# Optimization experiments

Measured on AMD Instinct MI355X. Metric: run time of the kernel, lower is better.

The kernel has to match this reference:

```python
import jax, jax.numpy as jnp
import numpy as np

EMBED_DIM = 512
NUM_HEADS = 8
HEAD_DIM = EMBED_DIM // NUM_HEADS
FACTOR = 5
B, T = 4, 2048


def setup_inputs() -> dict:
    key = jax.random.key(0)
    ks = jax.random.split(key, 10)
    s = EMBED_DIM ** -0.5
    hidden_states = jax.random.normal(ks[0], (B, T, EMBED_DIM), dtype=jnp.float32)
    log_L = int(np.ceil(np.log1p(T)))
    u_part = min(FACTOR * T * log_L, T)
    index_sample = jax.random.randint(ks[1], (u_part,), 0, T, dtype=jnp.int32)
    Wq = jax.random.normal(ks[2], (EMBED_DIM, EMBED_DIM), dtype=jnp.float32) * s
    bq = jnp.zeros((EMBED_DIM,), dtype=jnp.float32)
    Wk = jax.random.normal(ks[3], (EMBED_DIM, EMBED_DIM), dtype=jnp.float32) * s
    bk = jnp.zeros((EMBED_DIM,), dtype=jnp.float32)
    Wv = jax.random.normal(ks[4], (EMBED_DIM, EMBED_DIM), dtype=jnp.float32) * s
    bv = jnp.zeros((EMBED_DIM,), dtype=jnp.float32)
    Wo = jax.random.normal(ks[5], (EMBED_DIM, EMBED_DIM), dtype=jnp.float32) * s
    bo = jnp.zeros((EMBED_DIM,), dtype=jnp.float32)
    return {"hidden_states": hidden_states, "index_sample": index_sample,
            "Wq": Wq, "bq": bq, "Wk": Wk, "bk": bk, "Wv": Wv, "bv": bv,
            "Wo": Wo, "bo": bo}


def _split_heads(x, bsz, seqlen):
    # [B, T, E] -> [B*H, T, head_dim]
    return x.reshape(bsz, seqlen, NUM_HEADS, HEAD_DIM).transpose(0, 2, 1, 3).reshape(bsz * NUM_HEADS, seqlen, HEAD_DIM)


def reference(hidden_states, index_sample, Wq, bq, Wk, bk, Wv, bv, Wo, bo):
    bsz, tgt_len, embed_dim = hidden_states.shape
    scaling = HEAD_DIM ** -0.5
    q = (hidden_states @ Wq.T + bq) * scaling
    k = hidden_states @ Wk.T + bk
    v = hidden_states @ Wv.T + bv
    q = _split_heads(q, bsz, tgt_len)   # [BH, T, d]
    k = _split_heads(k, bsz, tgt_len)
    v = _split_heads(v, bsz, tgt_len)
    L_k = tgt_len
    log_q = int(np.ceil(np.log1p(tgt_len)))
    u = min(FACTOR * log_q, tgt_len)
    # random key sampling (indices precomputed, length u_part)
    k_sample = k[:, index_sample, :]                                  # [BH, u_part, d]
    qk_sample = jnp.einsum('bqd,bkd->bqk', q, k_sample)               # [BH, T, u_part]
    # sparsity measurement: max - mean over sampled keys (mean uses full L_k as in source)
    sparsity = qk_sample.max(axis=-1) - qk_sample.sum(axis=-1) / L_k  # [BH, T]
    top_idx = jax.lax.top_k(sparsity, u)[1]                           # [BH, u]
    q_reduce = jnp.take_along_axis(q, top_idx[:, :, None], axis=1)    # [BH, u, d]
    attn = jax.nn.softmax(jnp.einsum('bud,bkd->buk', q_reduce, k), axis=-1)  # [BH, u, L]
    attn_out = jnp.einsum('buk,bkd->bud', attn, v)                    # [BH, u, d]
    # encoder context: mean of values over time, scattered with active-query outputs
    context = jnp.broadcast_to(v.mean(axis=1, keepdims=True), v.shape)  # [BH, T, d]
    bh_idx = jnp.arange(bsz * NUM_HEADS)[:, None]
    context = context.at[bh_idx, top_idx].set(attn_out)
    out = context.reshape(bsz, NUM_HEADS, tgt_len, HEAD_DIM).transpose(0, 2, 1, 3).reshape(bsz, tgt_len, embed_dim)
    return out @ Wo.T + bo
```

## Files before the change

kernel.cpp:

```cpp
#include <hip/hip_runtime.h>
#include <hip/hip_bf16.h>
#include <math.h>

#define T_LEN 2048
#define EMB   512
#define NHEAD 8
#define HDIM  64
#define BHEADS 32
#define USEL  40

typedef __bf16 bf16v8 __attribute__((ext_vector_type(8)));
typedef _Float16 f16x8 __attribute__((ext_vector_type(8)));
typedef float f32x4 __attribute__((ext_vector_type(4)));
typedef unsigned short u16;

__device__ __forceinline__ void cvt4_hilo(const float4 f, uint2& ph, uint2& pl)
{
    __hip_bfloat16 h0 = __float2bfloat16(f.x);
    __hip_bfloat16 h1 = __float2bfloat16(f.y);
    __hip_bfloat16 h2 = __float2bfloat16(f.z);
    __hip_bfloat16 h3 = __float2bfloat16(f.w);
    __hip_bfloat16 l0 = __float2bfloat16(f.x - __bfloat162float(h0));
    __hip_bfloat16 l1 = __float2bfloat16(f.y - __bfloat162float(h1));
    __hip_bfloat16 l2 = __float2bfloat16(f.z - __bfloat162float(h2));
    __hip_bfloat16 l3 = __float2bfloat16(f.w - __bfloat162float(h3));
    ph.x = (unsigned)*(const u16*)&h0 | ((unsigned)*(const u16*)&h1 << 16);
    ph.y = (unsigned)*(const u16*)&h2 | ((unsigned)*(const u16*)&h3 << 16);
    pl.x = (unsigned)*(const u16*)&l0 | ((unsigned)*(const u16*)&l1 << 16);
    pl.y = (unsigned)*(const u16*)&l2 | ((unsigned)*(const u16*)&l3 << 16);
}

__device__ __forceinline__ void cvt4_hilo_h(const float4 f, uint2& ph, uint2& pl)
{
    _Float16 h0 = (_Float16)f.x;
    _Float16 h1 = (_Float16)f.y;
    _Float16 h2 = (_Float16)f.z;
    _Float16 h3 = (_Float16)f.w;
    _Float16 l0 = (_Float16)(f.x - (float)h0);
    _Float16 l1 = (_Float16)(f.y - (float)h1);
    _Float16 l2 = (_Float16)(f.z - (float)h2);
    _Float16 l3 = (_Float16)(f.w - (float)h3);
    ph.x = (unsigned)*(const u16*)&h0 | ((unsigned)*(const u16*)&h1 << 16);
    ph.y = (unsigned)*(const u16*)&h2 | ((unsigned)*(const u16*)&h3 << 16);
    pl.x = (unsigned)*(const u16*)&l0 | ((unsigned)*(const u16*)&l1 << 16);
    pl.y = (unsigned)*(const u16*)&l2 | ((unsigned)*(const u16*)&l3 << 16);
}

__device__ __forceinline__ void cvt1_hilo_h(float f, u16& h, u16& l)
{
    _Float16 hh = (_Float16)f;
    _Float16 ll = (_Float16)(f - (float)hh);
    h = *(const u16*)&hh;
    l = *(const u16*)&ll;
}

__global__ __launch_bounds__(256)
void pack_hilo_kernel(const float* __restrict__ X,
                      const float* __restrict__ Wq, const float* __restrict__ Wk,
                      const float* __restrict__ Wv, const float* __restrict__ Wo,
                      u16* __restrict__ Xp, u16* __restrict__ Wp)
{
    alignas(16) __shared__ u16 th[4096];
    alignas(16) __shared__ u16 tl[4096];
    const int b = blockIdx.x, tid = threadIdx.x;

    const float* src; u16* dst;
    if (b < 1024) {
        int mt = b >> 4, kt = b & 15;
        src = X + (size_t)(mt * 128) * EMB + kt * 32;
        dst = Xp + (size_t)b * 8192;
    } else {
        int wdx = b - 1024;
        int z = wdx >> 6, nt = (wdx >> 4) & 3, kt = wdx & 15;
        const float* W = (z == 0) ? Wq : (z == 1) ? Wk : (z == 2) ? Wv : Wo;
        src = W + (size_t)(nt * 128) * EMB + kt * 32;
        dst = Wp + (size_t)wdx * 8192;
    }

    #pragma unroll
    for (int s = 0; s < 4; ++s) {
        int u = tid + 256 * s;
        int row = u >> 3, c4 = u & 7;
        float4 f = *(const float4*)&src[(size_t)row * EMB + c4 * 4];
        uint2 ph, pl;
        cvt4_hilo_h(f, ph, pl);
        int kq = c4 >> 1, e4 = (c4 & 1) * 4;
        *(uint2*)&th[kq * 1024 + row * 8 + e4] = ph;
        *(uint2*)&tl[kq * 1024 + row * 8 + e4] = pl;
    }
    __syncthreads();

    uint4* d4 = (uint4*)dst;
    const uint4* s4h = (const uint4*)th;
    const uint4* s4l = (const uint4*)tl;
    d4[tid]       = s4h[tid];
    d4[tid + 256] = s4h[tid + 256];
    d4[tid + 512] = s4l[tid];
    d4[tid + 768] = s4l[tid + 256];
}

__global__ __launch_bounds__(256)
void qkv_mfma_kernel(const u16* __restrict__ Xp, const u16* __restrict__ Wp,
                     const float* __restrict__ bq, const float* __restrict__ bk,
                     const float* __restrict__ bv,
                     float* __restrict__ qo, float* __restrict__ ko, float* __restrict__ vo)
{
    alignas(16) __shared__ u16 Ah[2][4096];
    alignas(16) __shared__ u16 Al[2][4096];
    alignas(16) __shared__ u16 Bh[2][4096];
    alignas(16) __shared__ u16 Bl[2][4096];

    const int z = blockIdx.z;
    const float* bias; float* dst; float scale;
    if (z == 0)      { bias = bq; dst = qo; scale = 0.125f; }
    else if (z == 1) { bias = bk; dst = ko; scale = 1.0f;   }
    else             { bias = bv; dst = vo; scale = 1.0f;   }
    const bool three = (z != 2);

    const int tid = threadIdx.x;
    const int mt = blockIdx.x;
    const int nt = blockIdx.y;
    const int w = tid >> 6, lane = tid & 63;
    const int wm = w & 1, wn = w >> 1;
    const int lm = lane & 15, kq = lane >> 4;

    const u16* Abase = Xp + (size_t)mt * (16 * 8192);
    const u16* Bbase = Wp + (size_t)(z * 4 + nt) * (16 * 8192);

    f32x4 acc[4][4];
    #pragma unroll
    for (int i = 0; i < 4; ++i)
        #pragma unroll
        for (int j = 0; j < 4; ++j)
            #pragma unroll
            for (int r = 0; r < 4; ++r) acc[i][j][r] = 0.0f;

    auto stage = [&](int kt, int buf) {
        const u16* at = Abase + kt * 8192;
        const u16* bt = Bbase + kt * 8192;
        const u16* gsrc; u16* ldst;
        if (w == 0)      { gsrc = at;        ldst = &Ah[buf][0]; }
        else if (w == 1) { gsrc = at + 4096; ldst = &Al[buf][0]; }
        else if (w == 2) { gsrc = bt;        ldst = &Bh[buf][0]; }
        else             { gsrc = bt + 4096; ldst = &Bl[buf][0]; }
        if (three || (w & 1) == 0) {
            #pragma unroll
            for (int i = 0; i < 8; ++i)
                __builtin_amdgcn_global_load_lds(
                    (const __attribute__((address_space(1))) void*)(gsrc + (size_t)lane * 8 + i * 512),
                    (__attribute__((address_space(3))) void*)(ldst + i * 512),
                    16, 0, 0);
        }
    };

    stage(0, 0);

    for (int kt = 0; kt < 16; ++kt) {
        const int cur = kt & 1;
        if (kt + 1 < 16) {
            stage(kt + 1, cur ^ 1);
            asm volatile("s_waitcnt vmcnt(8)" ::: "memory");
        } else {
            asm volatile("s_waitcnt vmcnt(0)" ::: "memory");
        }
        __builtin_amdgcn_s_barrier();
        __builtin_amdgcn_sched_barrier(0);

        f16x8 ah[4], al[4], bh[4], bl[4];
        #pragma unroll
        for (int i = 0; i < 4; ++i) {
            int ar = (wm * 64 + i * 16 + lm) * 8 + kq * 1024;
            int br = (wn * 64 + i * 16 + lm) * 8 + kq * 1024;
            ah[i] = *(const f16x8*)&Ah[cur][ar];
            bh[i] = *(const f16x8*)&Bh[cur][br];
            if (three) {
                al[i] = *(const f16x8*)&Al[cur][ar];
                bl[i] = *(const f16x8*)&Bl[cur][br];
            }
        }
        #pragma unroll
        for (int i = 0; i < 4; ++i)
            #pragma unroll
            for (int j = 0; j < 4; ++j) {
                acc[i][j] = __builtin_amdgcn_mfma_f32_16x16x32_f16(ah[i], bh[j], acc[i][j], 0, 0, 0);
                if (three) {
                    acc[i][j] = __builtin_amdgcn_mfma_f32_16x16x32_f16(ah[i], bl[j], acc[i][j], 0, 0, 0);
                    acc[i][j] = __builtin_amdgcn_mfma_f32_16x16x32_f16(al[i], bh[j], acc[i][j], 0, 0, 0);
                }
            }
        __builtin_amdgcn_s_barrier();
    }

    #pragma unroll
    for (int j = 0; j < 4; ++j) {
        int ng = nt * 128 + wn * 64 + j * 16 + lm;
        int h = ng >> 6, d = ng & 63;
        float bv_ = bias[ng];
        #pragma unroll
        for (int i = 0; i < 4; ++i) {
            #pragma unroll
            for (int r = 0; r < 4; ++r) {
                int mg = mt * 128 + wm * 64 + i * 16 + kq * 4 + r;
                int b = mg >> 11, t = mg & 2047;
                dst[((size_t)((b * NHEAD + h) * T_LEN + t)) * HDIM + d] =
                    (acc[i][j][r] + bv_) * scale;
            }
        }
    }
}

__global__ __launch_bounds__(256)
void qkv_proj_kernel(const float* __restrict__ X,
                     const float* __restrict__ Wq, const float* __restrict__ bq,
                     const float* __restrict__ Wk, const float* __restrict__ bk,
                     const float* __restrict__ Wv, const float* __restrict__ bv,
                     float* __restrict__ qo, float* __restrict__ ko, float* __restrict__ vo)
{
    alignas(16) __shared__ u16 Ah[128 * 40];
    alignas(16) __shared__ u16 Al[128 * 40];
    alignas(16) __shared__ u16 Bh[128 * 40];
    alignas(16) __shared__ u16 Bl[128 * 40];

    const int z = blockIdx.z;
    const float* W; const float* bias; float* dst; float scale;
    if (z == 0)      { W = Wq; bias = bq; dst = qo; scale = 0.125f; }
    else if (z == 1) { W = Wk; bias = bk; dst = ko; scale = 1.0f;   }
    else             { W = Wv; bias = bv; dst = vo; scale = 1.0f;   }

    const int tid = threadIdx.x;
    const int m0 = blockIdx.x * 128;
    const int n0 = blockIdx.y * 128;
    const int w = tid >> 6, lane = tid & 63;
    const int wm = w & 1, wn = w >> 1;
    const int lm = lane & 15, kq = lane >> 4;

    f32x4 acc[4][4];
    #pragma unroll
    for (int i = 0; i < 4; ++i)
        #pragma unroll
        for (int j = 0; j < 4; ++j)
            #pragma unroll
            for (int r = 0; r < 4; ++r) acc[i][j][r] = 0.0f;

    for (int kc = 0; kc < EMB; kc += 32) {
        __syncthreads();
        #pragma unroll
        for (int s = 0; s < 4; ++s) {
            int u = tid + 256 * s;
            int row = u >> 3, c4 = u & 7;
            float4 fa = *(const float4*)&X[(size_t)(m0 + row) * EMB + kc + c4 * 4];
            float4 fb = *(const float4*)&W[(n0 + row) * EMB + kc + c4 * 4];
            uint2 ph, pl;
            cvt4_hilo_h(fa, ph, pl);
            *(uint2*)&Ah[row * 40 + c4 * 4] = ph;
            *(uint2*)&Al[row * 40 + c4 * 4] = pl;
            cvt4_hilo_h(fb, ph, pl);
            *(uint2*)&Bh[row * 40 + c4 * 4] = ph;
            *(uint2*)&Bl[row * 40 + c4 * 4] = pl;
        }
        __syncthreads();

        f16x8 ah[4], al[4], bh[4], bl[4];
        #pragma unroll
        for (int i = 0; i < 4; ++i) {
            int ra = (wm * 64 + i * 16 + lm) * 40 + kq * 8;
            ah[i] = *(const f16x8*)&Ah[ra];
            al[i] = *(const f16x8*)&Al[ra];
            int rb = (wn * 64 + i * 16 + lm) * 40 + kq * 8;
            bh[i] = *(const f16x8*)&Bh[rb];
            bl[i] = *(const f16x8*)&Bl[rb];
        }
        #pragma unroll
        for (int i = 0; i < 4; ++i)
            #pragma unroll
            for (int j = 0; j < 4; ++j) {
                acc[i][j] = __builtin_amdgcn_mfma_f32_16x16x32_f16(ah[i], bh[j], acc[i][j], 0, 0, 0);
                acc[i][j] = __builtin_amdgcn_mfma_f32_16x16x32_f16(ah[i], bl[j], acc[i][j], 0, 0, 0);
                acc[i][j] = __builtin_amdgcn_mfma_f32_16x16x32_f16(al[i], bh[j], acc[i][j], 0, 0, 0);
            }
    }

    #pragma unroll
    for (int j = 0; j < 4; ++j) {
        int ng = n0 + wn * 64 + j * 16 + lm;
        int h = ng >> 6, d = ng & 63;
        float bv_ = bias[ng];
        #pragma unroll
        for (int i = 0; i < 4; ++i) {
            #pragma unroll
            for (int r = 0; r < 4; ++r) {
                int mg = m0 + wm * 64 + i * 16 + kq * 4 + r;
                int b = mg >> 11, t = mg & 2047;
                dst[((size_t)((b * NHEAD + h) * T_LEN + t)) * HDIM + d] =
                    (acc[i][j][r] + bv_) * scale;
            }
        }
    }
}

__global__ __launch_bounds__(256)
void count_compact_kernel(const int* __restrict__ idxs, int n,
                          int* __restrict__ count, int* __restrict__ klist,
                          int* __restrict__ ncp)
{
    __shared__ int cnt[T_LEN];
    __shared__ int th_tot[256];
    __shared__ int th_off[256];
    __shared__ int ncs;
    const int tid = threadIdx.x;
    for (int j = tid; j < T_LEN; j += 256) cnt[j] = 0;
    __syncthreads();
    for (int i = tid; i < n; i += 256) atomicAdd(&cnt[idxs[i] & (T_LEN - 1)], 1);
    __syncthreads();
    const int base = tid * 8;
    int flags[8]; int loc = 0;
    #pragma unroll
    for (int j = 0; j < 8; ++j) {
        int c = cnt[base + j];
        count[base + j] = c;
        flags[j] = (c > 0); loc += flags[j];
    }
    th_tot[tid] = loc;
    __syncthreads();
    if (tid == 0) {
        int run = 0;
        for (int i = 0; i < 256; ++i) { th_off[i] = run; run += th_tot[i]; }
        ncs = run;
        ncp[0] = run;
    }
    __syncthreads();
    int off = th_off[tid];
    #pragma unroll
    for (int j = 0; j < 8; ++j)
        if (flags[j]) klist[off++] = base + j;
    __syncthreads();
    const int nc = ncs;
    const int nt = (nc + 127) & ~127;
    const int k0 = klist[0];
    for (int j = nc + tid; j < nt; j += 256) klist[j] = k0;
}

__global__ __launch_bounds__(256)
void ksum_vmean_part_kernel(const int* __restrict__ count,
                            const float* __restrict__ k, const float* __restrict__ v,
                            float* __restrict__ kpart, float* __restrict__ vpart)
{
    __shared__ int cs[256];
    alignas(16) __shared__ float rk[16 * 64];
    alignas(16) __shared__ float rv[16 * 64];

    const int sl = blockIdx.x, bh = blockIdx.y, tid = threadIdx.x;
    const int f4 = tid & 15, tg = tid >> 4;
    const int t0 = sl * 256;

    cs[tid] = count[t0 + tid];
    __syncthreads();

    const float4* k4 = (const float4*)(k + (size_t)bh * T_LEN * HDIM) + t0 * 16;
    const float4* v4 = (const float4*)(v + (size_t)bh * T_LEN * HDIM) + t0 * 16;

    float4 ak = {0.f, 0.f, 0.f, 0.f}, av = {0.f, 0.f, 0.f, 0.f};
    #pragma unroll
    for (int s = 0; s < 16; ++s) {
        int t = tg + s * 16;
        float c = (float)cs[t];
        float4 kf = k4[t * 16 + f4];
        float4 vf = v4[t * 16 + f4];
        ak.x = fmaf(c, kf.x, ak.x); ak.y = fmaf(c, kf.y, ak.y);
        ak.z = fmaf(c, kf.z, ak.z); ak.w = fmaf(c, kf.w, ak.w);
        av.x += vf.x; av.y += vf.y; av.z += vf.z; av.w += vf.w;
    }
    *(float4*)&rk[tg * 64 + f4 * 4] = ak;
    *(float4*)&rv[tg * 64 + f4 * 4] = av;
    __syncthreads();

    if (tid < 64) {
        float sk = 0.f, sv = 0.f;
        #pragma unroll
        for (int g = 0; g < 16; ++g) { sk += rk[g * 64 + tid]; sv += rv[g * 64 + tid]; }
        kpart[((size_t)bh * 8 + sl) * 64 + tid] = sk;
        vpart[((size_t)bh * 8 + sl) * 64 + tid] = sv;
    }
}

__global__ __launch_bounds__(64)
void ksum_vmean_reduce_kernel(const float* __restrict__ kpart, const float* __restrict__ vpart,
                              float* __restrict__ ksum, float* __restrict__ vmean)
{
    const int bh = blockIdx.x, d = threadIdx.x;
    float sk = 0.f, sv = 0.f;
    #pragma unroll
    for (int sl = 0; sl < 8; ++sl) {
        sk += kpart[((size_t)bh * 8 + sl) * 64 + d];
        sv += vpart[((size_t)bh * 8 + sl) * 64 + d];
    }
    ksum[bh * 64 + d]  = sk;
    vmean[bh * 64 + d] = sv * (1.0f / 2048.0f);
}

__global__ __launch_bounds__(256)
void pack_k_kernel(const float* __restrict__ k, const int* __restrict__ klist,
                   const int* __restrict__ ncp, u16* __restrict__ Kp)
{
    alignas(16) __shared__ u16 th[8192];
    alignas(16) __shared__ u16 tl[8192];
    const int wg = blockIdx.x, tid = threadIdx.x;
    const int swz = (wg & 7) * 64 + (wg >> 3);
    const int bh = swz >> 4, kt = swz & 15;
    const int ntiles = (ncp[0] + 127) >> 7;
    if (kt >= ntiles) return;

    const float4* kb4 = (const float4*)(k + (size_t)bh * T_LEN * HDIM);
    #pragma unroll
    for (int s = 0; s < 8; ++s) {
        int u = tid + 256 * s;
        int row = u >> 4, c4 = u & 15;
        int krow = klist[kt * 128 + row];
        float4 f = kb4[krow * 16 + c4];
        uint2 ph, pl;
        cvt4_hilo_h(f, ph, pl);
        int base = (c4 >> 3) * 4096 + ((c4 >> 1) & 3) * 1024 + row * 8 + (c4 & 1) * 4;
        *(uint2*)&th[base] = ph;
        *(uint2*)&tl[base] = pl;
    }
    __syncthreads();

    u16* dst = Kp + ((size_t)bh * 16 + kt) * 16384;
    uint4* d4 = (uint4*)dst;
    const uint4* s4h = (const uint4*)th;
    const uint4* s4l = (const uint4*)tl;
    #pragma unroll
    for (int i = 0; i < 4; ++i) d4[tid + 256 * i] = s4h[tid + 256 * i];
    #pragma unroll
    for (int i = 0; i < 4; ++i) d4[1024 + tid + 256 * i] = s4l[tid + 256 * i];
}

__global__ __launch_bounds__(256)
void sparsity_scan_kernel(const float* __restrict__ q, const u16* __restrict__ Kp,
                          const float* __restrict__ ksum,
                          const int* __restrict__ ncp, float* __restrict__ spars)
{
    alignas(16) __shared__ u16 KH[10240];
    alignas(16) __shared__ u16 KL[10240];
    __shared__ float ksm[64];
    __shared__ float smax[128];
    __shared__ float sdotL[128];

    const int tid = threadIdx.x;
    const int wg = blockIdx.x;
    const int swz = (wg & 7) * 64 + (wg >> 3);
    const int bh = swz >> 4;
    const int q0 = (swz & 15) * 128;
    const int w = tid >> 6, lane = tid & 63;
    const int lm = lane & 15, kq = lane >> 4;

    const float* qb = q + ((size_t)bh * T_LEN + q0) * HDIM;
    const int ntiles = (ncp[0] + 127) >> 7;

    if (tid < 64) ksm[tid] = ksum[bh * 64 + tid];

    #pragma unroll
    for (int s = 0; s < 8; ++s) {
        int u = tid + 256 * s;
        int row = u >> 4, c4 = u & 15;
        float4 f = *(const float4*)&qb[row * HDIM + c4 * 4];
        uint2 ph, pl;
        cvt4_hilo_h(f, ph, pl);
        int base = ((c4 >> 3) * 128 + row) * 40 + (c4 & 7) * 4;
        *(uint2*)&KH[base] = ph;
        *(uint2*)&KL[base] = pl;
    }
    __syncthreads();

    f16x8 qh[2][2], ql[2][2];
    #pragma unroll
    for (int i = 0; i < 2; ++i)
        #pragma unroll
        for (int c = 0; c < 2; ++c) {
            int ra = (c * 128 + w * 32 + i * 16 + lm) * 40 + kq * 8;
            qh[i][c] = *(const f16x8*)&KH[ra];
            ql[i][c] = *(const f16x8*)&KL[ra];
        }

    {
        float4 k0a = *(const float4*)&ksm[kq * 8];
        float4 k0b = *(const float4*)&ksm[kq * 8 + 4];
        float4 k1a = *(const float4*)&ksm[32 + kq * 8];
        float4 k1b = *(const float4*)&ksm[32 + kq * 8 + 4];
        float kmv[2][8] = {{k0a.x, k0a.y, k0a.z, k0a.w, k0b.x, k0b.y, k0b.z, k0b.w},
                           {k1a.x, k1a.y, k1a.z, k1a.w, k1b.x, k1b.y, k1b.z, k1b.w}};
        #pragma unroll
        for (int i = 0; i < 2; ++i) {
            float sd = 0.f;
            #pragma unroll
            for (int c = 0; c < 2; ++c)
                #pragma unroll
                for (int e = 0; e < 8; ++e)
                    sd = fmaf((float)qh[i][c][e] + (float)ql[i][c][e], kmv[c][e], sd);
            sd += __shfl_xor(sd, 16, 64);
            sd += __shfl_xor(sd, 32, 64);
            if (kq == 0) sdotL[w * 32 + i * 16 + lm] = sd;
        }
    }

    float vmax[2][4];
    #pragma unroll
    for (int i = 0; i < 2; ++i)
        #pragma unroll
        for (int r = 0; r < 4; ++r) vmax[i][r] = -INFINITY;

    const u16* kpb = Kp + (size_t)bh * (16 * 16384);

    for (int kt = 0; kt < ntiles; ++kt) {
        __syncthreads();
        const u16* kp = kpb + kt * 16384;
        const u16* gsrc; u16* ldst;
        if (w == 0)      { gsrc = kp;         ldst = KH; }
        else if (w == 1) { gsrc = kp + 4096;  ldst = KH + 4096; }
        else if (w == 2) { gsrc = kp + 8192;  ldst = KL; }
        else             { gsrc = kp + 12288; ldst = KL + 4096; }
        #pragma unroll
        for (int i = 0; i < 8; ++i)
            __builtin_amdgcn_global_load_lds(
                (const __attribute__((address_space(1))) void*)(gsrc + (size_t)lane * 8 + i * 512),
                (__attribute__((address_space(3))) void*)(ldst + i * 512),
                16, 0, 0);
        __syncthreads();

        #pragma unroll
        for (int j = 0; j < 8; ++j) {
            int rb0 = kq * 1024 + (j * 16 + lm) * 8;
            int rb1 = 4096 + kq * 1024 + (j * 16 + lm) * 8;
            f16x8 bh0 = *(const f16x8*)&KH[rb0];
            f16x8 bl0 = *(const f16x8*)&KL[rb0];
            f16x8 bh1 = *(const f16x8*)&KH[rb1];
            f16x8 bl1 = *(const f16x8*)&KL[rb1];
            f32x4 a0 = {0.f, 0.f, 0.f, 0.f};
            f32x4 a1 = {0.f, 0.f, 0.f, 0.f};
            a0 = __builtin_amdgcn_mfma_f32_16x16x32_f16(qh[0][0], bh0, a0, 0, 0, 0);
            a1 = __builtin_amdgcn_mfma_f32_16x16x32_f16(qh[1][0], bh0, a1, 0, 0, 0);
            a0 = __builtin_amdgcn_mfma_f32_16x16x32_f16(qh[0][0], bl0, a0, 0, 0, 0);
            a1 = __builtin_amdgcn_mfma_f32_16x16x32_f16(qh[1][0], bl0, a1, 0, 0, 0);
            a0 = __builtin_amdgcn_mfma_f32_16x16x32_f16(ql[0][0], bh0, a0, 0, 0, 0);
            a1 = __builtin_amdgcn_mfma_f32_16x16x32_f16(ql[1][0], bh0, a1, 0, 0, 0);
            a0 = __builtin_amdgcn_mfma_f32_16x16x32_f16(qh[0][1], bh1, a0, 0, 0, 0);
            a1 = __builtin_amdgcn_mfma_f32_16x16x32_f16(qh[1][1], bh1, a1, 0, 0, 0);
            a0 = __builtin_amdgcn_mfma_f32_16x16x32_f16(qh[0][1], bl1, a0, 0, 0, 0);
            a1 = __builtin_amdgcn_mfma_f32_16x16x32_f16(qh[1][1], bl1, a1, 0, 0, 0);
            a0 = __builtin_amdgcn_mfma_f32_16x16x32_f16(ql[0][1], bh1, a0, 0, 0, 0);
            a1 = __builtin_amdgcn_mfma_f32_16x16x32_f16(ql[1][1], bh1, a1, 0, 0, 0);
            #pragma unroll
            for (int r = 0; r < 4; ++r) {
                vmax[0][r] = fmaxf(vmax[0][r], a0[r]);
                vmax[1][r] = fmaxf(vmax[1][r], a1[r]);
            }
        }
    }

    #pragma unroll
    for (int i = 0; i < 2; ++i)
        #pragma unroll
        for (int r = 0; r < 4; ++r) {
            float m = vmax[i][r];
            m = fmaxf(m, __shfl_xor(m, 1, 64));
            m = fmaxf(m, __shfl_xor(m, 2, 64));
            m = fmaxf(m, __shfl_xor(m, 4, 64));
            m = fmaxf(m, __shfl_xor(m, 8, 64));
            if (lm == 0) smax[w * 32 + i * 16 + kq * 4 + r] = m;
        }
    __syncthreads();

    if (tid < 128)
        spars[bh * T_LEN + q0 + tid] = smax[tid] - sdotL[tid] * (1.0f / 2048.0f);
}

__global__ __launch_bounds__(256)
void sparsity_scan_fb_kernel(const float* __restrict__ q, const float* __restrict__ k,
                             const float* __restrict__ ksum, const int* __restrict__ klist,
                             const int* __restrict__ ncp, float* __restrict__ spars)
{
    alignas(16) __shared__ u16 KH[256 * 40];
    alignas(16) __shared__ u16 KL[256 * 40];
    __shared__ float ksm[64];
    __shared__ float smax[128];
    __shared__ float sdotL[128];

    const int tid = threadIdx.x;
    const int bh = blockIdx.y;
    const int q0 = blockIdx.x * 128;
    const int w = tid >> 6, lane = tid & 63;
    const int lm = lane & 15, kq = lane >> 4;

    const float* qb = q + ((size_t)bh * T_LEN + q0) * HDIM;
    const float4* kb4 = (const float4*)(k + (size_t)bh * T_LEN * HDIM);
    const int ntiles = (ncp[0] + 127) >> 7;

    if (tid < 64) ksm[tid] = ksum[bh * 64 + tid];

    #pragma unroll
    for (int s = 0; s < 8; ++s) {
        int u = tid + 256 * s;
        int row = u >> 4, c4 = u & 15;
        float4 f = *(const float4*)&qb[row * HDIM + c4 * 4];
        uint2 ph, pl;
        cvt4_hilo_h(f, ph, pl);
        int base = ((c4 >> 3) * 128 + row) * 40 + (c4 & 7) * 4;
        *(uint2*)&KH[base] = ph;
        *(uint2*)&KL[base] = pl;
    }
    __syncthreads();

    f16x8 qh[2][2], ql[2][2];
// ... 141 lines not shown
        const int A = (tid == 255) ? 0 : sfx[tid + 1];
        const int here = sfx[tid];
        __syncthreads();
        if (A < need && here >= need) {
            sh_bin = tid;
            sh_need = need - A;
        }
        __syncthreads();
        kpref |= (unsigned)sh_bin << shift;
        shift -= 8;
    }

    const unsigned K = kpref;
    const int need_eq = sh_need;

    #pragma unroll
    for (int s = 0; s < 8; ++s) {
        int j = tid + 256 * s;
        unsigned kk = keys[j];
        if (kk > K) {
            int pos = atomicAdd(&nsel, 1);
            if (pos < USEL) topi[bh * USEL + pos] = j;
        } else if (kk == K) {
            atomicAdd(&neq, 1);
        }
    }
    __syncthreads();
    const int base = nsel;
    const int E = neq;
    __syncthreads();

    if (E == need_eq) {
        #pragma unroll
        for (int s = 0; s < 8; ++s) {
            int j = tid + 256 * s;
            if (keys[j] == K) {
                int pos = atomicAdd(&cnt2, 1);
                if (base + pos < USEL) topi[bh * USEL + base + pos] = j;
            }
        }
    } else {
        #pragma unroll
        for (int s = 0; s < 8; ++s) {
            int j = tid + 256 * s;
            if (keys[j] == K) {
                int rank = 0;
                for (int j2 = 0; j2 < j; ++j2) rank += (keys[j2] == K);
                if (rank < need_eq && base + rank < USEL)
                    topi[bh * USEL + base + rank] = j;
            }
        }
    }
}

__global__ __launch_bounds__(256)
void gather_q_kernel(const float* __restrict__ q, const int* __restrict__ topi,
                     float* __restrict__ qsel)
{
    const int bh = blockIdx.x, tid = threadIdx.x;
    for (int i = tid; i < USEL * HDIM; i += 256) {
        int u = i >> 6, d = i & 63;
        int t = topi[bh * USEL + u] & (T_LEN - 1);
        qsel[(size_t)bh * USEL * HDIM + i] = q[((size_t)bh * T_LEN + t) * HDIM + d];
    }
}

__global__ __launch_bounds__(256)
void sel_scores_direct_kernel(const float* __restrict__ q, const float* __restrict__ k,
                              const int* __restrict__ topi, float* __restrict__ S)
{
    __shared__ float qsT[64 * 41];
    __shared__ float ksT[64 * 257];

    const int sl = blockIdx.x, bh = blockIdx.y, tid = threadIdx.x;
    const int t0 = sl * 256;

    for (int i = tid; i < USEL * HDIM; i += 256) {
        int u = i >> 6, d = i & 63;
        int t = topi[bh * USEL + u] & (T_LEN - 1);
        qsT[d * 41 + u] = q[((size_t)bh * T_LEN + t) * HDIM + d];
    }
    const float4* k4 = (const float4*)(k + (size_t)bh * T_LEN * HDIM);
    #pragma unroll
    for (int s = 0; s < 16; ++s) {
        int u = tid + 256 * s;
        int c4 = u & 15, t = u >> 4;
        float4 f = k4[(t0 + t) * 16 + c4];
        ksT[(c4 * 4 + 0) * 257 + t] = f.x;
        ksT[(c4 * 4 + 1) * 257 + t] = f.y;
        ksT[(c4 * 4 + 2) * 257 + t] = f.z;
        ksT[(c4 * 4 + 3) * 257 + t] = f.w;
    }
    __syncthreads();

    const int qg = tid >> 5;
    const int kg = tid & 31;

    float acc[5][8];
    #pragma unroll
    for (int i = 0; i < 5; ++i)
        #pragma unroll
        for (int j = 0; j < 8; ++j) acc[i][j] = 0.0f;

    #pragma unroll 4
    for (int d = 0; d < 64; ++d) {
        float qv[5], kv[8];
        #pragma unroll
        for (int i = 0; i < 5; ++i) qv[i] = qsT[d * 41 + qg * 5 + i];
        #pragma unroll
        for (int j = 0; j < 8; ++j) kv[j] = ksT[d * 257 + kg + 32 * j];
        #pragma unroll
        for (int i = 0; i < 5; ++i)
            #pragma unroll
            for (int j = 0; j < 8; ++j)
                acc[i][j] = fmaf(qv[i], kv[j], acc[i][j]);
    }

    #pragma unroll
    for (int i = 0; i < 5; ++i) {
        float* sp = &S[((size_t)bh * USEL + qg * 5 + i) * T_LEN + t0 + kg];
        #pragma unroll
        for (int j = 0; j < 8; ++j) sp[32 * j] = acc[i][j];
    }
}

__global__ __launch_bounds__(256)
void sel_scores_kernel(const float* __restrict__ qsel, const float* __restrict__ k,
                       float* __restrict__ S)
{
    __shared__ float qsT[64 * 41];
    __shared__ float ksT[64 * 257];

    const int sl = blockIdx.x, bh = blockIdx.y, tid = threadIdx.x;
    const int t0 = sl * 256;

    for (int i = tid; i < USEL * HDIM; i += 256) {
        int u = i >> 6, d = i & 63;
        qsT[d * 41 + u] = qsel[(size_t)bh * USEL * HDIM + i];
    }
    const float4* k4 = (const float4*)(k + (size_t)bh * T_LEN * HDIM);
    #pragma unroll
    for (int s = 0; s < 16; ++s) {
        int u = tid + 256 * s;
        int c4 = u & 15, t = u >> 4;
        float4 f = k4[(t0 + t) * 16 + c4];
        ksT[(c4 * 4 + 0) * 257 + t] = f.x;
        ksT[(c4 * 4 + 1) * 257 + t] = f.y;
        ksT[(c4 * 4 + 2) * 257 + t] = f.z;
        ksT[(c4 * 4 + 3) * 257 + t] = f.w;
    }
    __syncthreads();

    const int qg = tid >> 5;
    const int kg = tid & 31;

    float acc[5][8];
    #pragma unroll
    for (int i = 0; i < 5; ++i)
        #pragma unroll
        for (int j = 0; j < 8; ++j) acc[i][j] = 0.0f;

    #pragma unroll 4
    for (int d = 0; d < 64; ++d) {
        float qv[5], kv[8];
        #pragma unroll
        for (int i = 0; i < 5; ++i) qv[i] = qsT[d * 41 + qg * 5 + i];
        #pragma unroll
        for (int j = 0; j < 8; ++j) kv[j] = ksT[d * 257 + kg + 32 * j];
        #pragma unroll
        for (int i = 0; i < 5; ++i)
            #pragma unroll
            for (int j = 0; j < 8; ++j)
                acc[i][j] = fmaf(qv[i], kv[j], acc[i][j]);
    }

    #pragma unroll
    for (int i = 0; i < 5; ++i) {
        float* sp = &S[((size_t)bh * USEL + qg * 5 + i) * T_LEN + t0 + kg];
        #pragma unroll
        for (int j = 0; j < 8; ++j) sp[32 * j] = acc[i][j];
    }
}

__global__ __launch_bounds__(256)
void sel_softmax_kernel(float* __restrict__ S)
{
    __shared__ float red[256];
    const int row = blockIdx.x, tid = threadIdx.x;
    float* sr = S + (size_t)row * T_LEN;

    float x[8];
    float m = -INFINITY;
    #pragma unroll
    for (int s = 0; s < 8; ++s) { x[s] = sr[tid + 256 * s]; m = fmaxf(m, x[s]); }
    red[tid] = m;
    __syncthreads();
    for (int s = 128; s > 0; s >>= 1) {
        if (tid < s) red[tid] = fmaxf(red[tid], red[tid + s]);
        __syncthreads();
    }
    m = red[0];
    __syncthreads();

    float sum = 0.f;
    #pragma unroll
    for (int s = 0; s < 8; ++s) { x[s] = __expf(x[s] - m); sum += x[s]; }
    red[tid] = sum;
    __syncthreads();
    for (int s = 128; s > 0; s >>= 1) {
        if (tid < s) red[tid] += red[tid + s];
        __syncthreads();
    }
    float inv = 1.0f / red[0];
    #pragma unroll
    for (int s = 0; s < 8; ++s) sr[tid + 256 * s] = x[s] * inv;
}

__global__ __launch_bounds__(256)
void pv_part_kernel(const float* __restrict__ S, const float* __restrict__ v,
                    float* __restrict__ part)
{
    __shared__ float ps[USEL * 128];
    __shared__ float vs[128 * 69];
    __shared__ float obuf[128 * 20];

    const int sl = blockIdx.x, bh = blockIdx.y, tid = threadIdx.x;
    const int t0 = sl * 128;

    for (int i = tid; i < USEL * 128; i += 256) {
        int q = i >> 7, t = i & 127;
        ps[q * 128 + t] = S[((size_t)bh * USEL + q) * T_LEN + t0 + t];
    }
    const float4* v4 = (const float4*)(v + (size_t)bh * T_LEN * HDIM);
    #pragma unroll
    for (int s = 0; s < 8; ++s) {
        int u = tid + 256 * s;
        int c4 = u & 15, t = u >> 4;
        float4 f = v4[(t0 + t) * 16 + c4];
        vs[t * 69 + c4 * 4 + 0] = f.x;
        vs[t * 69 + c4 * 4 + 1] = f.y;
        vs[t * 69 + c4 * 4 + 2] = f.z;
        vs[t * 69 + c4 * 4 + 3] = f.w;
    }
    __syncthreads();

    const int qg = tid >> 5, r = tid & 31;
    const int dg = r >> 1, th = r & 1;
    const int tb = th * 64;

    float o[5][4];
    #pragma unroll
    for (int i = 0; i < 5; ++i)
        #pragma unroll
        for (int j = 0; j < 4; ++j) o[i][j] = 0.0f;

    #pragma unroll 4
    for (int tt = 0; tt < 64; ++tt) {
        int t = tb + tt;
        float pv[5];
        #pragma unroll
        for (int i = 0; i < 5; ++i) pv[i] = ps[(qg * 5 + i) * 128 + t];
        float4 vv = *(const float4*)&vs[t * 69 + dg * 4];
        #pragma unroll
        for (int i = 0; i < 5; ++i) {
            o[i][0] = fmaf(pv[i], vv.x, o[i][0]);
            o[i][1] = fmaf(pv[i], vv.y, o[i][1]);
            o[i][2] = fmaf(pv[i], vv.z, o[i][2]);
            o[i][3] = fmaf(pv[i], vv.w, o[i][3]);
        }
    }

    const int p = qg * 16 + dg;
    if (th == 1) {
        #pragma unroll
        for (int i = 0; i < 5; ++i)
            #pragma unroll
            for (int j = 0; j < 4; ++j) obuf[p * 20 + i * 4 + j] = o[i][j];
    }
    __syncthreads();
    if (th == 0) {
        float* pb = part + ((size_t)bh * 16 + sl) * (USEL * HDIM);
        #pragma unroll
        for (int i = 0; i < 5; ++i)
            #pragma unroll
            for (int j = 0; j < 4; ++j)
                pb[(qg * 5 + i) * HDIM + dg * 4 + j] = o[i][j] + obuf[p * 20 + i * 4 + j];
    }
}

__global__ __launch_bounds__(256)
void pv_merge_kernel(const float* __restrict__ part, float* __restrict__ attn)
{
    const int bh = blockIdx.x, tid = threadIdx.x;
    for (int i = tid; i < USEL * HDIM; i += 256) {
        float s = 0.f;
        #pragma unroll
        for (int sl = 0; sl < 16; ++sl)
            s += part[((size_t)bh * 16 + sl) * (USEL * HDIM) + i];
        attn[(size_t)bh * USEL * HDIM + i] = s;
    }
}

__global__ __launch_bounds__(256)
void ctx_build_pack_kernel(const float* __restrict__ vmean,
                           const float* __restrict__ part,
                           const int* __restrict__ topi,
                           u16* __restrict__ CXp)
{
    const int tile = blockIdx.x;
    const int tid = threadIdx.x;
    const int mt = tile >> 4, kt = tile & 15;
    const int b = mt >> 4, h = kt >> 1;
    const int bh = (b << 3) | h;
    const int dbase = (kt & 1) * 32;
    const int ttile = mt & 15;

    uint4 vh[4], vl[4];
    #pragma unroll
    for (int kq = 0; kq < 4; ++kq) {
        unsigned hw[4], lw[4];
        #pragma unroll
        for (int p = 0; p < 4; ++p) {
            u16 h0, l0, h1, l1;
            cvt1_hilo_h(vmean[bh * 64 + dbase + kq * 8 + p * 2],     h0, l0);
            cvt1_hilo_h(vmean[bh * 64 + dbase + kq * 8 + p * 2 + 1], h1, l1);
            hw[p] = (unsigned)h0 | ((unsigned)h1 << 16);
            lw[p] = (unsigned)l0 | ((unsigned)l1 << 16);
        }
        vh[kq] = make_uint4(hw[0], hw[1], hw[2], hw[3]);
        vl[kq] = make_uint4(lw[0], lw[1], lw[2], lw[3]);
    }
    u16* dst = CXp + (size_t)tile * 8192;
    uint4* dh = (uint4*)dst;
    uint4* dl = (uint4*)(dst + 4096);
    #pragma unroll
    for (int s = 0; s < 2; ++s) {
        int u = tid + 256 * s;
        dh[u] = vh[u >> 7];
        dl[u] = vl[u >> 7];
    }
    __syncthreads();

    for (int i = tid; i < USEL * 32; i += 256) {
        int u = i >> 5, c = i & 31;
        int t = topi[bh * USEL + u] & (T_LEN - 1);
        if ((t >> 7) != ttile) continue;
        int row = t & 127;
        int d = dbase + c;
        float s = 0.f;
        #pragma unroll
        for (int sl = 0; sl < 16; ++sl)
            s += part[((size_t)bh * 16 + sl) * (USEL * HDIM) + u * 64 + d];
        u16 hh, ll;
        cvt1_hilo_h(s, hh, ll);
        u16* base = dst + (c >> 3) * 1024 + row * 8 + (c & 7);
        base[0]    = hh;
        base[4096] = ll;
    }
}

__global__ __launch_bounds__(256)
void out_mfma_kernel(const u16* __restrict__ CXp, const u16* __restrict__ Wp,
                     const float* __restrict__ bo, float* __restrict__ out)
{
    alignas(16) __shared__ u16 Ah[2][4096];
    alignas(16) __shared__ u16 Al[2][4096];
    alignas(16) __shared__ u16 Bh[2][4096];
    alignas(16) __shared__ u16 Bl[2][4096];

    const int tid = threadIdx.x;
    const int mt = blockIdx.x;
    const int nt = blockIdx.y;
    const int w = tid >> 6, lane = tid & 63;
    const int wm = w & 1, wn = w >> 1;
    const int lm = lane & 15, kq = lane >> 4;

    const u16* Abase = CXp + (size_t)mt * (16 * 8192);
    const u16* Bbase = Wp + (size_t)(3 * 4 + nt) * (16 * 8192);

    f32x4 acc[4][4];
    #pragma unroll
    for (int i = 0; i < 4; ++i)
        #pragma unroll
        for (int j = 0; j < 4; ++j)
            #pragma unroll
            for (int r = 0; r < 4; ++r) acc[i][j][r] = 0.0f;

    auto stage = [&](int kt, int buf) {
        const u16* at = Abase + kt * 8192;
        const u16* bt = Bbase + kt * 8192;
        const u16* gsrc; u16* ldst;
        if (w == 0)      { gsrc = at;        ldst = &Ah[buf][0]; }
        else if (w == 1) { gsrc = at + 4096; ldst = &Al[buf][0]; }
        else if (w == 2) { gsrc = bt;        ldst = &Bh[buf][0]; }
        else             { gsrc = bt + 4096; ldst = &Bl[buf][0]; }
        #pragma unroll
        for (int i = 0; i < 8; ++i)
            __builtin_amdgcn_global_load_lds(
                (const __attribute__((address_space(1))) void*)(gsrc + (size_t)lane * 8 + i * 512),
                (__attribute__((address_space(3))) void*)(ldst + i * 512),
                16, 0, 0);
    };

    stage(0, 0);

    for (int kt = 0; kt < 16; ++kt) {
        const int cur = kt & 1;
        if (kt + 1 < 16) {
            stage(kt + 1, cur ^ 1);
            asm volatile("s_waitcnt vmcnt(8)" ::: "memory");
        } else {
            asm volatile("s_waitcnt vmcnt(0)" ::: "memory");
        }
        __builtin_amdgcn_s_barrier();
        __builtin_amdgcn_sched_barrier(0);

        f16x8 ah[4], al[4], bh[4], bl[4];
        #pragma unroll
        for (int i = 0; i < 4; ++i) {
            int ar = (wm * 64 + i * 16 + lm) * 8 + kq * 1024;
            int br = (wn * 64 + i * 16 + lm) * 8 + kq * 1024;
            ah[i] = *(const f16x8*)&Ah[cur][ar];
            al[i] = *(const f16x8*)&Al[cur][ar];
            bh[i] = *(const f16x8*)&Bh[cur][br];
            bl[i] = *(const f16x8*)&Bl[cur][br];
        }
        #pragma unroll
        for (int i = 0; i < 4; ++i)
            #pragma unroll
            for (int j = 0; j < 4; ++j) {
                acc[i][j] = __builtin_amdgcn_mfma_f32_16x16x32_f16(ah[i], bh[j], acc[i][j], 0, 0, 0);
                acc[i][j] = __builtin_amdgcn_mfma_f32_16x16x32_f16(ah[i], bl[j], acc[i][j], 0, 0, 0);
                acc[i][j] = __builtin_amdgcn_mfma_f32_16x16x32_f16(al[i], bh[j], acc[i][j], 0, 0, 0);
            }
        __builtin_amdgcn_s_barrier();
    }

    #pragma unroll
    for (int j = 0; j < 4; ++j) {
        int ng = nt * 128 + wn * 64 + j * 16 + lm;
        float bias = bo[ng];
        #pragma unroll
        for (int i = 0; i < 4; ++i)
            #pragma unroll
            for (int r = 0; r < 4; ++r) {
                int mg = mt * 128 + wm * 64 + i * 16 + kq * 4 + r;
                out[(size_t)mg * EMB + ng] = acc[i][j][r] + bias;
            }
    }
}

__global__ __launch_bounds__(256)
void ctx_fill_kernel(const float* __restrict__ vmean, float* __restrict__ ctx)
{
    int flat = blockIdx.x * 256 + threadIdx.x;
    int d = flat & 63, h = (flat >> 6) & 7, b = flat >> 20;
    int bh = (b << 3) | h;
    ctx[flat] = vmean[bh * 64 + d];
}

__global__ void ctx_scatter_kernel(const float* __restrict__ attn, const int* __restrict__ topi,
                                   float* __restrict__ ctx)
{
    const int u = blockIdx.x, bh = blockIdx.y, d = threadIdx.x;
    const int b = bh >> 3, h = bh & 7;
    const int t = topi[bh * USEL + u] & (T_LEN - 1);
    ctx[(size_t)(b * T_LEN + t) * EMB + h * 64 + d] =
        attn[((size_t)bh * USEL + u) * HDIM + d];
}

__global__ __launch_bounds__(256)
void out_proj_kernel(const float* __restrict__ A, const float* __restrict__ Wo,
                     const float* __restrict__ bo, float* __restrict__ out)
{
    alignas(16) __shared__ u16 Ah[128 * 40];
    alignas(16) __shared__ u16 Al[128 * 40];
    alignas(16) __shared__ u16 Bh[128 * 40];
    alignas(16) __shared__ u16 Bl[128 * 40];

    const int tid = threadIdx.x;
    const int m0 = blockIdx.x * 128;
    const int n0 = blockIdx.y * 128;
    const int w = tid >> 6, lane = tid & 63;
    const int wm = w & 1, wn = w >> 1;
    const int lm = lane & 15, kq = lane >> 4;

    f32x4 acc[4][4];
    #pragma unroll
    for (int i = 0; i < 4; ++i)
        #pragma unroll
        for (int j = 0; j < 4; ++j)
            #pragma unroll
            for (int r = 0; r < 4; ++r) acc[i][j][r] = 0.0f;

    for (int kc = 0; kc < EMB; kc += 32) {
        __syncthreads();
        #pragma unroll
        for (int s = 0; s < 4; ++s) {
            int u = tid + 256 * s;
            int row = u >> 3, c4 = u & 7;
            float4 fa = *(const float4*)&A[(size_t)(m0 + row) * EMB + kc + c4 * 4];
            float4 fb = *(const float4*)&Wo[(n0 + row) * EMB + kc + c4 * 4];
            uint2 ph, pl;
            cvt4_hilo(fa, ph, pl);
            *(uint2*)&Ah[row * 40 + c4 * 4] = ph;
            *(uint2*)&Al[row * 40 + c4 * 4] = pl;
            cvt4_hilo(fb, ph, pl);
            *(uint2*)&Bh[row * 40 + c4 * 4] = ph;
            *(uint2*)&Bl[row * 40 + c4 * 4] = pl;
        }
        __syncthreads();

        bf16v8 ah[4], al[4], bh[4], bl[4];
        #pragma unroll
        for (int i = 0; i < 4; ++i) {
            int ra = (wm * 64 + i * 16 + lm) * 40 + kq * 8;
            ah[i] = *(const bf16v8*)&Ah[ra];
            al[i] = *(const bf16v8*)&Al[ra];
            int rb = (wn * 64 + i * 16 + lm) * 40 + kq * 8;
            bh[i] = *(const bf16v8*)&Bh[rb];
            bl[i] = *(const bf16v8*)&Bl[rb];
        }
        #pragma unroll
        for (int i = 0; i < 4; ++i)
            #pragma unroll
            for (int j = 0; j < 4; ++j) {
                acc[i][j] = __builtin_amdgcn_mfma_f32_16x16x32_bf16(ah[i], bh[j], acc[i][j], 0, 0, 0);
                acc[i][j] = __builtin_amdgcn_mfma_f32_16x16x32_bf16(ah[i], bl[j], acc[i][j], 0, 0, 0);
                acc[i][j] = __builtin_amdgcn_mfma_f32_16x16x32_bf16(al[i], bh[j], acc[i][j], 0, 0, 0);
            }
    }

    #pragma unroll
    for (int j = 0; j < 4; ++j) {
        int ng = n0 + wn * 64 + j * 16 + lm;
        float bias = bo[ng];
        #pragma unroll
        for (int i = 0; i < 4; ++i)
            #pragma unroll
            for (int r = 0; r < 4; ++r) {
                int mg = m0 + wm * 64 + i * 16 + kq * 4 + r;
                out[(size_t)mg * EMB + ng] = acc[i][j][r] + bias;
            }
    }
}

__global__ __launch_bounds__(256)
void ws_diag_kernel(float* __restrict__ out, int n, float mib)
{
    int flat = blockIdx.x * 256 + threadIdx.x;
    if (flat < n) out[flat] = mib;
}

extern "C" void kernel_launch(void* const* d_in, const int* in_sizes, int n_in,
                              void* d_out, int out_size, void* d_ws, size_t ws_size,
                              hipStream_t stream)
{
    const float* X = nullptr; const int* idxs = nullptr;
    const float* Wseen[4] = {nullptr, nullptr, nullptr, nullptr};
    const float* bseen[4] = {nullptr, nullptr, nullptr, nullptr};
    int nw = 0, nb = 0, u_part = 2048;
    for (int i = 0; i < n_in; ++i) {
        int sz = in_sizes[i];
        if (sz == EMB * EMB * 16) { if (!X) X = (const float*)d_in[i]; }
        else if (sz == T_LEN)     { if (!idxs) { idxs = (const int*)d_in[i]; u_part = sz; } }
        else if (sz == EMB * EMB) { if (nw < 4) Wseen[nw++] = (const float*)d_in[i]; }
        else if (sz == EMB)       { if (nb < 4) bseen[nb++] = (const float*)d_in[i]; }
    }
    if (!X || !idxs || nw < 4 || nb < 4) {
        X = (const float*)d_in[0]; idxs = (const int*)d_in[1];
        Wseen[0] = (const float*)d_in[2]; bseen[0] = (const float*)d_in[3];
        Wseen[1] = (const float*)d_in[4]; bseen[1] = (const float*)d_in[5];
        Wseen[2] = (const float*)d_in[6]; bseen[2] = (const float*)d_in[7];
        Wseen[3] = (const float*)d_in[8]; bseen[3] = (const float*)d_in[9];
        u_part = in_sizes[1];
    }
    const float *Wq = Wseen[0], *Wk = Wseen[1], *Wv = Wseen[2], *Wo = Wseen[3];
    const float *bq = bseen[0], *bk = bseen[1], *bv = bseen[2], *bo = bseen[3];

    const size_t NEED      = 50951168ULL;
    const size_t XP_B      = 16777216ULL;
    const size_t WP_B      = 4194304ULL;
    const size_t CXP_B     = 16777216ULL;
    const size_t S_B       = 10485760ULL;
    const size_t PVP_B     = 5242880ULL;
    const size_t NEED_BIG  = NEED + XP_B + WP_B + CXP_B + S_B + PVP_B;
    if (ws_size < NEED) {
        ws_diag_kernel<<<(out_size + 255) / 256, 256, 0, stream>>>(
            (float*)d_out, out_size, (float)(ws_size >> 20));
        return;
    }

    float* ws    = (float*)d_ws;
    float* qw    = ws;
    float* kw    = qw + 4194304;
    float* vw    = kw + 4194304;
    float* tail  = vw + 4194304;
    float* slotA = tail;
    float* spars = tail + 81920;
    int*   count = (int*)(tail + 147456);
    float* ksum  = tail + 149504;
    float* vmean = tail + 151552;
    int*   topi  = (int*)(tail + 153600);
    float* kpart = tail;
    float* vpart = tail + 16384;
    int*   klist = (int*)(tail + 32768);
    int*   ncp   = (int*)(tail + 34816);
    float* Sfb   = qw;
    float* pvpfb = qw + 2621440;
    float* qsel  = slotA;
    float* attn  = slotA;
    float* ctx   = (float*)d_ws;
    u16*   Xp    = (u16*)((char*)d_ws + NEED);
    u16*   Wp    = (u16*)((char*)d_ws + NEED + XP_B);
    u16*   CXp   = (u16*)((char*)d_ws + NEED + XP_B + WP_B);
    float* S2    = (float*)((char*)d_ws + NEED + XP_B + WP_B + CXP_B);
    float* pvp2  = S2 + 2621440;
    u16*   Kp    = Xp;

    const bool big = (ws_size >= NEED_BIG);

    if (big) {
        pack_hilo_kernel<<<1280, 256, 0, stream>>>(X, Wq, Wk, Wv, Wo, Xp, Wp);
        qkv_mfma_kernel<<<dim3(64, 4, 3), 256, 0, stream>>>(Xp, Wp, bq, bk, bv, qw, kw, vw);
    } else {
        qkv_proj_kernel<<<dim3(64, 4, 3), 256, 0, stream>>>(X, Wq, bq, Wk, bk, Wv, bv, qw, kw, vw);
    }
    count_compact_kernel<<<1, 256, 0, stream>>>(idxs, u_part, count, klist, ncp);
    ksum_vmean_part_kernel<<<dim3(8, 32), 256, 0, stream>>>(count, kw, vw, kpart, vpart);
    ksum_vmean_reduce_kernel<<<32, 64, 0, stream>>>(kpart, vpart, ksum, vmean);
    if (big) {
        pack_k_kernel<<<512, 256, 0, stream>>>(kw, klist, ncp, Kp);
        sparsity_scan_kernel<<<512, 256, 0, stream>>>(qw, Kp, ksum, ncp, spars);
    } else {
        sparsity_scan_fb_kernel<<<dim3(16, 32), 256, 0, stream>>>(qw, kw, ksum, klist, ncp, spars);
    }
    topk_kernel<<<32, 256, 0, stream>>>(spars, topi);
    if (big) {
        sel_scores_direct_kernel<<<dim3(8, 32), 256, 0, stream>>>(qw, kw, topi, S2);
        sel_softmax_kernel<<<1280, 256, 0, stream>>>(S2);
        pv_part_kernel<<<dim3(16, 32), 256, 0, stream>>>(S2, vw, pvp2);
        ctx_build_pack_kernel<<<1024, 256, 0, stream>>>(vmean, pvp2, topi, CXp);
        out_mfma_kernel<<<dim3(64, 4), 256, 0, stream>>>(CXp, Wp, bo, (float*)d_out);
    } else {
        gather_q_kernel<<<32, 256, 0, stream>>>(qw, topi, qsel);
        sel_scores_kernel<<<dim3(8, 32), 256, 0, stream>>>(qsel, kw, Sfb);
        sel_softmax_kernel<<<1280, 256, 0, stream>>>(Sfb);
        pv_part_kernel<<<dim3(16, 32), 256, 0, stream>>>(Sfb, vw, pvpfb);
        pv_merge_kernel<<<32, 256, 0, stream>>>(pvpfb, attn);
        ctx_fill_kernel<<<16384, 256, 0, stream>>>(vmean, ctx);
        ctx_scatter_kernel<<<dim3(USEL, BHEADS), 64, 0, stream>>>(attn, topi, ctx);
        out_proj_kernel<<<dim3(64, 4), 256, 0, stream>>>(ctx, Wo, bo, (float*)d_out);
    }
}
```

Baseline: 266.9 us.

## Fuse count-weighted K sum and V sum into QKV GEMM epilogue

```diff
diff --git a/kernel.cpp b/kernel.cpp
--- a/kernel.cpp
+++ b/kernel.cpp
@@ -102,13 +102,16 @@
 __global__ __launch_bounds__(256)
 void qkv_mfma_kernel(const u16* __restrict__ Xp, const u16* __restrict__ Wp,
                      const float* __restrict__ bq, const float* __restrict__ bk,
-                     const float* __restrict__ bv,
+                     const float* __restrict__ bv, const int* __restrict__ count,
+                     float* __restrict__ ksum, float* __restrict__ vsum,
                      float* __restrict__ qo, float* __restrict__ ko, float* __restrict__ vo)
 {
     alignas(16) __shared__ u16 Ah[2][4096];
     alignas(16) __shared__ u16 Al[2][4096];
     alignas(16) __shared__ u16 Bh[2][4096];
     alignas(16) __shared__ u16 Bl[2][4096];
+    __shared__ float cbuf[128];
+    __shared__ float red[128];
 
     const int z = blockIdx.z;
     const float* bias; float* dst; float scale;
@@ -205,6 +208,44 @@
                 dst[((size_t)((b * NHEAD + h) * T_LEN + t)) * HDIM + d] =
                     (acc[i][j][r] + bv_) * scale;
             }
+        }
+    }
+
+    if (z != 0) {
+        const int b = mt >> 4;
+        if (tid < 128)
+            cbuf[tid] = (z == 1) ? (float)count[(mt & 15) * 128 + tid] : 1.0f;
+        __syncthreads();
+
+        float part[4];
+        #pragma unroll
+        for (int j = 0; j < 4; ++j) {
+            float bias_j = bias[nt * 128 + wn * 64 + j * 16 + lm];
+            float p = 0.f;
+            #pragma unroll
+            for (int i = 0; i < 4; ++i)
+                #pragma unroll
+                for (int r = 0; r < 4; ++r)
+                    p += cbuf[wm * 64 + i * 16 + kq * 4 + r] * (acc[i][j][r] + bias_j);
+            p += __shfl_xor(p, 16, 64);
+            p += __shfl_xor(p, 32, 64);
+            part[j] = p;
+        }
+        if (kq == 0 && wm == 0) {
+            #pragma unroll
+            for (int j = 0; j < 4; ++j) red[wn * 64 + j * 16 + lm] = part[j];
+        }
+        __syncthreads();
+        if (kq == 0 && wm == 1) {
+            #pragma unroll
+            for (int j = 0; j < 4; ++j) red[wn * 64 + j * 16 + lm] += part[j];
+        }
+        __syncthreads();
+        if (tid < 128) {
+            int ng = nt * 128 + tid;
+            int h = ng >> 6, d = ng & 63;
+            float* dstp = (z == 1) ? ksum : vsum;
+            atomicAdd(&dstp[(b * 8 + h) * 64 + d], red[tid]);
         }
     }
 }
@@ -301,13 +342,15 @@
 __global__ __launch_bounds__(256)
 void count_compact_kernel(const int* __restrict__ idxs, int n,
                           int* __restrict__ count, int* __restrict__ klist,
-                          int* __restrict__ ncp)
+                          int* __restrict__ ncp,
+                          float* __restrict__ ksumz, float* __restrict__ vsumz)
 {
     __shared__ int cnt[T_LEN];
     __shared__ int th_tot[256];
     __shared__ int th_off[256];
     __shared__ int ncs;
     const int tid = threadIdx.x;
+    for (int j = tid; j < BHEADS * HDIM; j += 256) { ksumz[j] = 0.f; vsumz[j] = 0.f; }
     for (int j = tid; j < T_LEN; j += 256) cnt[j] = 0;
     __syncthreads();
     for (int i = tid; i < n; i += 256) atomicAdd(&cnt[idxs[i] & (T_LEN - 1)], 1);
@@ -1055,7 +1098,7 @@
 }
 
 __global__ __launch_bounds__(256)
-void ctx_build_pack_kernel(const float* __restrict__ vmean,
+void ctx_build_pack_kernel(const float* __restrict__ vsum,
                            const float* __restrict__ part,
                            const int* __restrict__ topi,
                            u16* __restrict__ CXp)
@@ -1075,8 +1118,8 @@
         #pragma unroll
         for (int p = 0; p < 4; ++p) {
             u16 h0, l0, h1, l1;
-            cvt1_hilo_h(vmean[bh * 64 + dbase + kq * 8 + p * 2],     h0, l0);
-            cvt1_hilo_h(vmean[bh * 64 + dbase + kq * 8 + p * 2 + 1], h1, l1);
+            cvt1_hilo_h(vsum[bh * 64 + dbase + kq * 8 + p * 2]     * (1.0f / 2048.0f), h0, l0);
+            cvt1_hilo_h(vsum[bh * 64 + dbase + kq * 8 + p * 2 + 1] * (1.0f / 2048.0f), h1, l1);
             hw[p] = (unsigned)h0 | ((unsigned)h1 << 16);
             lw[p] = (unsigned)l0 | ((unsigned)l1 << 16);
         }
@@ -1373,29 +1416,27 @@
 
     const bool big = (ws_size >= NEED_BIG);
 
+    count_compact_kernel<<<1, 256, 0, stream>>>(idxs, u_part, count, klist, ncp,
+                                                ksum, vmean);
     if (big) {
         pack_hilo_kernel<<<1280, 256, 0, stream>>>(X, Wq, Wk, Wv, Wo, Xp, Wp);
-        qkv_mfma_kernel<<<dim3(64, 4, 3), 256, 0, stream>>>(Xp, Wp, bq, bk, bv, qw, kw, vw);
-    } else {
-        qkv_proj_kernel<<<dim3(64, 4, 3), 256, 0, stream>>>(X, Wq, bq, Wk, bk, Wv, bv, qw, kw, vw);
-    }
-    count_compact_kernel<<<1, 256, 0, stream>>>(idxs, u_part, count, klist, ncp);
-    ksum_vmean_part_kernel<<<dim3(8, 32), 256, 0, stream>>>(count, kw, vw, kpart, vpart);
-    ksum_vmean_reduce_kernel<<<32, 64, 0, stream>>>(kpart, vpart, ksum, vmean);
-    if (big) {
+        qkv_mfma_kernel<<<dim3(64, 4, 3), 256, 0, stream>>>(Xp, Wp, bq, bk, bv,
+                                                            count, ksum, vmean,
+                                                            qw, kw, vw);
         pack_k_kernel<<<512, 256, 0, stream>>>(kw, klist, ncp, Kp);
         sparsity_scan_kernel<<<512, 256, 0, stream>>>(qw, Kp, ksum, ncp, spars);
-    } else {
-        sparsity_scan_fb_kernel<<<dim3(16, 32), 256, 0, stream>>>(qw, kw, ksum, klist, ncp, spars);
-    }
-    topk_kernel<<<32, 256, 0, stream>>>(spars, topi);
-    if (big) {
+        topk_kernel<<<32, 256, 0, stream>>>(spars, topi);
         sel_scores_direct_kernel<<<dim3(8, 32), 256, 0, stream>>>(qw, kw, topi, S2);
         sel_softmax_kernel<<<1280, 256, 0, stream>>>(S2);
         pv_part_kernel<<<dim3(16, 32), 256, 0, stream>>>(S2, vw, pvp2);
         ctx_build_pack_kernel<<<1024, 256, 0, stream>>>(vmean, pvp2, topi, CXp);
         out_mfma_kernel<<<dim3(64, 4), 256, 0, stream>>>(CXp, Wp, bo, (float*)d_out);
     } else {
+        qkv_proj_kernel<<<dim3(64, 4, 3), 256, 0, stream>>>(X, Wq, bq, Wk, bk, Wv, bv, qw, kw, vw);
+        ksum_vmean_part_kernel<<<dim3(8, 32), 256, 0, stream>>>(count, kw, vw, kpart, vpart);
+        ksum_vmean_reduce_kernel<<<32, 64, 0, stream>>>(kpart, vpart, ksum, vmean);
+        sparsity_scan_fb_kernel<<<dim3(16, 32), 256, 0, stream>>>(qw, kw, ksum, klist, ncp, spars);
+        topk_kernel<<<32, 256, 0, stream>>>(spars, topi);
         gather_q_kernel<<<32, 256, 0, stream>>>(qw, topi, qsel);
         sel_scores_kernel<<<dim3(8, 32), 256, 0, stream>>>(qsel, kw, Sfb);
         sel_softmax_kernel<<<1280, 256, 0, stream>>>(Sfb);
```

Result: slower. 277.2 us (+3.9%).
